# Optimization experiments

Hardware: AMD Instinct MI355X
Metric: run time of the kernel (lower is better)

Reference implementation:

```python
import jax, jax.numpy as jnp
import numpy as np

B, S, U, H = 4, 1024, 1024, 16
D = U // H  # d_k = 64


def setup_inputs() -> dict:
    key = jax.random.key(0)
    ks = jax.random.split(key, 11)
    f = lambda k, sh: jax.random.normal(k, sh, dtype=jnp.float32) * 0.02
    # causal multiplicative mask, as commonly passed to this module
    mask = jnp.broadcast_to(jnp.tril(jnp.ones((S, S), jnp.float32)), (B, S, S))
    return {
        "query": f(ks[0], (B, S, U)),
        "key": f(ks[1], (B, S, U)),
        "value": f(ks[2], (B, S, U)),
        "mask": mask,
        "Wq": f(ks[3], (U, U)), "bq": jnp.zeros((U,), jnp.float32),
        "Wk": f(ks[4], (U, U)), "bk": jnp.zeros((U,), jnp.float32),
        "Wv": f(ks[5], (U, U)), "bv": jnp.zeros((U,), jnp.float32),
        "Wo": f(ks[6], (U, U)), "bo": jnp.zeros((U,), jnp.float32),
    }


def reference(query, key, value, mask, Wq, bq, Wk, bk, Wv, bv, Wo, bo):
    scale = 1.0 / np.sqrt(D).astype(np.float32)
    # project and split heads: torch's split(d_k,dim=2)+cat(dim=0) == reshape [B,S,H,D]
    def heads(x, W, b):
        return (x @ W + b).reshape(B, S, H, D)
    q = heads(query, Wq, bq)
    k = heads(key, Wk, bk)
    v = heads(value, Wv, bv)
    A = jnp.einsum('bqhd,bkhd->bhqk', q, k) * scale  # [B,H,S,S]
    m = mask[:, None, :, :]  # broadcast over heads (== mask.repeat(n_heads,1,1))
    A = A * m - 1e10 * (1.0 - m)  # multiplicative + additive masking
    A = jax.nn.softmax(A, axis=-1)
    # dropout p=0.0 -> identity
    out = jnp.einsum('bhqk,bkhd->bqhd', A, v).reshape(B, S, U)
    return out @ Wo + bo
```

## Files before the change

kernel.cpp:

```cpp
#include <hip/hip_runtime.h>
#include <hip/hip_bf16.h>

typedef unsigned short u16;
typedef __attribute__((ext_vector_type(8))) short bf16x8;
typedef __attribute__((ext_vector_type(4))) float f32x4;
constexpr size_t M1 = 1024 * 1024;

static __device__ __forceinline__ float bf2f(u16 u) {
    return __uint_as_float(((unsigned)u) << 16);
}
static __device__ __forceinline__ u16 f2bf(float f) {
    __hip_bfloat16 h = __float2bfloat16(f);
    return *reinterpret_cast<u16*>(&h);
}
static __device__ __forceinline__ void g2lds16(const void* g, void* l) {
    __builtin_amdgcn_global_load_lds(
        (const __attribute__((address_space(1))) unsigned int*)g,
        (__attribute__((address_space(3))) unsigned int*)l, 16, 0, 0);
}
static __device__ __forceinline__ f32x4 mfma16(bf16x8 a, bf16x8 b, f32x4 c) {
    return __builtin_amdgcn_mfma_f32_16x16x32_bf16(a, b, c, 0, 0, 0);
}
static __device__ __forceinline__ bf16x8 ldfrag(const u16* base, int chunk) {
    return *(const bf16x8*)((const char*)base + (size_t)chunk * 16);
}
static __device__ __forceinline__ float fexp2(float x) {
    return __builtin_amdgcn_exp2f(x);
}

__global__ void sniff_kernel(const u16* __restrict__ q, int* __restrict__ flag) {
    const int i = threadIdx.x;
    const int e = (q[i] >> 7) & 0xFF;
    const unsigned long long m = __ballot(e >= 130);
    if (i == 0) *flag = (__popcll(m) >= 2) ? 1 : 0;
}

struct CastArgs { const float* src[2]; u16* dst[2]; int nChunks; };

__global__ __launch_bounds__(256) void cast_bf16(CastArgs ca, const int* __restrict__ flag) {
    if (*flag == 0) return;
    const int total = ca.nChunks;
    for (int c = blockIdx.x * 256 + threadIdx.x; c < total; c += gridDim.x * 256) {
        const int t = c >> 19;
        const size_t off = (size_t)(c & 524287);
        const float4 v0 = *((const float4*)ca.src[t] + off * 2);
        const float4 v1 = *((const float4*)ca.src[t] + off * 2 + 1);
        int4 v; u16* pv = (u16*)&v;
        pv[0] = f2bf(v0.x); pv[1] = f2bf(v0.y); pv[2] = f2bf(v0.z); pv[3] = f2bf(v0.w);
        pv[4] = f2bf(v1.x); pv[5] = f2bf(v1.y); pv[6] = f2bf(v1.z); pv[7] = f2bf(v1.w);
        *((int4*)ca.dst[t] + off) = v;
    }
}

struct T4 { const void* src[4]; u16* dst[4]; };

__global__ __launch_bounds__(256) void transpose64(
    T4 ta, const int* __restrict__ flag, int xRaw)
{
    __shared__ u16 Ts[64][72];
    const void* src = ta.src[blockIdx.z];
    u16* dst = ta.dst[blockIdx.z];
    const int tid = threadIdx.x;
    const int r0 = blockIdx.x * 64;
    const int c0 = blockIdx.y * 64;
    const bool f = xRaw && (*flag != 0);
#pragma unroll
    for (int i = 0; i < 4; ++i) {
        const int idx = tid + i * 256;
        const int r = idx >> 4, c4 = (idx & 15) * 4;
        if (f) {
            const float4 v = *(const float4*)((const float*)src + (size_t)(r0 + r) * 1024 + c0 + c4);
            Ts[r][c4 + 0] = f2bf(v.x); Ts[r][c4 + 1] = f2bf(v.y);
            Ts[r][c4 + 2] = f2bf(v.z); Ts[r][c4 + 3] = f2bf(v.w);
        } else {
            const ushort4 v = *(const ushort4*)((const u16*)src + (size_t)(r0 + r) * 1024 + c0 + c4);
            Ts[r][c4 + 0] = v.x; Ts[r][c4 + 1] = v.y;
            Ts[r][c4 + 2] = v.z; Ts[r][c4 + 3] = v.w;
        }
    }
    __syncthreads();
#pragma unroll
    for (int i = 0; i < 4; ++i) {
        const int idx = tid + i * 256;
        const int r = idx >> 4, c4 = (idx & 15) * 4;
        ushort4 o;
        o.x = Ts[c4 + 0][r]; o.y = Ts[c4 + 1][r];
        o.z = Ts[c4 + 2][r]; o.w = Ts[c4 + 3][r];
        *(ushort4*)(dst + (size_t)(c0 + r) * 1024 + r0 + c4) = o;
    }
}

struct G1 { const void* X; const u16* Xc; const u16* Wt; const void* Bias; void* Y; int yMode; };
struct G3 { G1 g[3]; };

union GS8 {
    struct { u16 A[2][2][128 * 64]; u16 B[2][2][128 * 64]; } st;
    u16 C[256 * 256];
};

__global__ __launch_bounds__(512, 2) void gemm256(
    G3 args, const int* __restrict__ flag)
{
    __shared__ __align__(16) GS8 sm;
    const G1 g = args.g[blockIdx.z];
    const bool f = (*flag != 0);
    const bool regA = f && (g.Xc == nullptr);
    const int tid = threadIdx.x;
    const int lane = tid & 63, w = tid >> 6;
    const int quad = lane >> 4, l16 = lane & 15;
    const int wr = w >> 2, wc = w & 3;
    const int rowBase = blockIdx.x * 256, colBase = blockIdx.y * 256;

    const u16* Xb = f ? g.Xc : (const u16*)g.X;
    const float* Xf = (const float*)g.X;

    f32x4 acc[8][4];
#pragma unroll
    for (int i = 0; i < 8; ++i)
#pragma unroll
        for (int j = 0; j < 4; ++j)
            acc[i][j] = f32x4{0.f, 0.f, 0.f, 0.f};

    auto stA = [&](int bf2, int h, int T2) {
        if (!regA) {
#pragma unroll
            for (int c = 0; c < 2; ++c) {
                const int l = c * 512 + tid;
                const int r  = ((l >> 6) << 3) | (l & 7);
                const int kc = (l >> 3) & 7;
                g2lds16(Xb + (size_t)(rowBase + h * 128 + r) * 1024 + T2 * 64 + kc * 8,
                        (char*)sm.st.A[bf2][h] + (size_t)l * 16);
            }
        } else {
#pragma unroll
            for (int c = 0; c < 2; ++c) {
                const int l = c * 512 + tid;
                const int r  = ((l >> 6) << 3) | (l & 7);
                const int kc = (l >> 3) & 7;
                const float* p = Xf + (size_t)(rowBase + h * 128 + r) * 1024 + T2 * 64 + kc * 8;
                const float4 v0 = *(const float4*)p;
                const float4 v1 = *(const float4*)(p + 4);
                int4 v; u16* pv = (u16*)&v;
                pv[0] = f2bf(v0.x); pv[1] = f2bf(v0.y); pv[2] = f2bf(v0.z); pv[3] = f2bf(v0.w);
                pv[4] = f2bf(v1.x); pv[5] = f2bf(v1.y); pv[6] = f2bf(v1.z); pv[7] = f2bf(v1.w);
                *(int4*)((char*)sm.st.A[bf2][h] + (size_t)l * 16) = v;
            }
            __builtin_amdgcn_s_waitcnt(0xC07F);
        }
    };
    auto stB = [&](int bf2, int h, int T2) {
#pragma unroll
        for (int c = 0; c < 2; ++c) {
            const int l = c * 512 + tid;
            const int r  = ((l >> 6) << 3) | (l & 7);
            const int kc = (l >> 3) & 7;
            g2lds16(g.Wt + (size_t)(colBase + h * 128 + r) * 1024 + T2 * 64 + kc * 8,
                    (char*)sm.st.B[bf2][h] + (size_t)l * 16);
        }
    };

    stA(0, 0, 0); stA(0, 1, 0); stB(0, 0, 0); stB(0, 1, 0);
    stA(1, 0, 1); stA(1, 1, 1); stB(1, 0, 1); stB(1, 1, 1);
    if (regA) __builtin_amdgcn_s_waitcnt(0x0074);
    else      __builtin_amdgcn_s_waitcnt(0x0078);
    __builtin_amdgcn_s_barrier();

    bf16x8 a[4][2], b[4][2];
    const int rbB = (wc & 1) * 64;

#pragma unroll 1
    for (int T = 0; T < 16; ++T) {
        const int buf = T & 1, nb = buf ^ 1;
        const u16* Ab = sm.st.A[buf][wr];
        const u16* Bb = sm.st.B[buf][wc >> 1];

#pragma unroll
        for (int i = 0; i < 4; ++i)
#pragma unroll
            for (int ks = 0; ks < 2; ++ks) {
                const int rl = i * 16 + l16;
                a[i][ks] = ldfrag(Ab, ((rl >> 3) << 6) | ((ks * 4 + quad) << 3) | (rl & 7));
            }
#pragma unroll
        for (int j = 0; j < 2; ++j)
#pragma unroll
            for (int ks = 0; ks < 2; ++ks) {
                const int rl = rbB + j * 16 + l16;
                b[j][ks] = ldfrag(Bb, ((rl >> 3) << 6) | ((ks * 4 + quad) << 3) | (rl & 7));
            }
        if (T >= 1 && T <= 14) stA(nb, 0, T + 1);
        __builtin_amdgcn_s_barrier();
        __builtin_amdgcn_s_setprio(1);
#pragma unroll
        for (int ks = 0; ks < 2; ++ks)
#pragma unroll
            for (int i = 0; i < 4; ++i)
#pragma unroll
                for (int j = 0; j < 2; ++j)
                    acc[i][j] = mfma16(a[i][ks], b[j][ks], acc[i][j]);
        __builtin_amdgcn_s_setprio(0);
        __builtin_amdgcn_s_barrier();

#pragma unroll
        for (int j = 2; j < 4; ++j)
#pragma unroll
            for (int ks = 0; ks < 2; ++ks) {
                const int rl = rbB + j * 16 + l16;
                b[j][ks] = ldfrag(Bb, ((rl >> 3) << 6) | ((ks * 4 + quad) << 3) | (rl & 7));
            }
        if (T >= 1 && T <= 14) stA(nb, 1, T + 1);
        __builtin_amdgcn_s_barrier();
        __builtin_amdgcn_s_setprio(1);
#pragma unroll
        for (int ks = 0; ks < 2; ++ks)
#pragma unroll
            for (int i = 0; i < 4; ++i)
#pragma unroll
                for (int j = 2; j < 4; ++j)
                    acc[i][j] = mfma16(a[i][ks], b[j][ks], acc[i][j]);
        __builtin_amdgcn_s_setprio(0);
        __builtin_amdgcn_s_barrier();

#pragma unroll
        for (int i = 0; i < 4; ++i)
#pragma unroll
            for (int ks = 0; ks < 2; ++ks) {
                const int rl = (i + 4) * 16 + l16;
                a[i][ks] = ldfrag(Ab, ((rl >> 3) << 6) | ((ks * 4 + quad) << 3) | (rl & 7));
            }
        if (T <= 13) stB(buf, 0, T + 2);
        __builtin_amdgcn_s_barrier();
        __builtin_amdgcn_s_setprio(1);
#pragma unroll
        for (int ks = 0; ks < 2; ++ks)
#pragma unroll
            for (int i = 0; i < 4; ++i)
#pragma unroll
                for (int j = 2; j < 4; ++j)
                    acc[i + 4][j] = mfma16(a[i][ks], b[j][ks], acc[i + 4][j]);
        __builtin_amdgcn_s_setprio(0);
        __builtin_amdgcn_s_barrier();

        if (T <= 13) stB(buf, 1, T + 2);
        __builtin_amdgcn_s_barrier();
        __builtin_amdgcn_s_setprio(1);
#pragma unroll
        for (int ks = 0; ks < 2; ++ks)
#pragma unroll
            for (int i = 0; i < 4; ++i)
#pragma unroll
                for (int j = 0; j < 2; ++j)
                    acc[i + 4][j] = mfma16(a[i][ks], b[j][ks], acc[i + 4][j]);
        __builtin_amdgcn_s_setprio(0);
        if (T < 14) __builtin_amdgcn_s_waitcnt(0x0074);
        else        __builtin_amdgcn_s_waitcnt(0x0070);
        __builtin_amdgcn_s_barrier();
    }

    const bool yf = (g.yMode == 2) && f;
    if (yf) {
#pragma unroll
        for (int j = 0; j < 4; ++j) {
            const int col = colBase + wc * 64 + j * 16 + l16;
            const float bv = ((const float*)g.Bias)[col];
#pragma unroll
            for (int i = 0; i < 8; ++i)
#pragma unroll
                for (int reg = 0; reg < 4; ++reg) {
                    const int row = rowBase + wr * 128 + i * 16 + quad * 4 + reg;
                    ((float*)g.Y)[(size_t)row * 1024 + col] = acc[i][j][reg] + bv;
                }
        }
        return;
    }

    __syncthreads();
    const bool vmode = (g.yMode == 1);
#pragma unroll
    for (int j = 0; j < 4; ++j) {
        const int cl = wc * 64 + j * 16 + l16;
        const float bv = f ? ((const float*)g.Bias)[colBase + cl]
                           : bf2f(((const u16*)g.Bias)[colBase + cl]);
#pragma unroll
        for (int i = 0; i < 8; ++i)
#pragma unroll
            for (int reg = 0; reg < 4; ++reg) {
                const int rl = wr * 128 + i * 16 + quad * 4 + reg;
                const int R = vmode ? cl : rl;
                const int Cc = vmode ? rl : cl;
                const int idx = R * 256 + ((((Cc >> 3) ^ (R & 31)) << 3) | (Cc & 7));
                sm.C[idx] = f2bf(acc[i][j][reg] + bv);
            }
    }
    __syncthreads();

    const int rr = tid >> 1, half = tid & 1;
    u16* dst;
    if (vmode) {
        const int bb = rowBase >> 10, s0 = rowBase & 1023;
        dst = (u16*)g.Y + (size_t)bb * M1 + (size_t)(colBase + rr) * 1024 + s0 + half * 128;
    } else {
        dst = (u16*)g.Y + (size_t)(rowBase + rr) * 1024 + colBase + half * 128;
    }
#pragma unroll
    for (int k2 = 0; k2 < 16; ++k2) {
        const int chunk = half * 16 + k2;
        const int4 v = *(const int4*)(sm.C + rr * 256 + ((chunk ^ (rr & 31)) << 3));
        *(int4*)(dst + k2 * 8) = v;
    }
}

union GSMem {
    struct { u16 A[3][128 * 32]; u16 B[3][128 * 32]; } st;
    u16 C[128 * 128];
};

__global__ __launch_bounds__(256) void gemm_mfma(
    G3 args, const int* __restrict__ flag, int xRaw)
{
    __shared__ __align__(16) GSMem sm;
    const G1 g = args.g[blockIdx.z];
    const bool f  = (*flag != 0);
    const bool xf = xRaw && f;
    const int tid = threadIdx.x;
    const int lane = tid & 63, w = tid >> 6;
    const int quad = lane >> 4, l16 = lane & 15;
    const int wm = (w & 1) * 64, wn = (w >> 1) * 64;
    const int rowBase = blockIdx.x * 128, colBase = blockIdx.y * 128;

    const u16* Xp = (const u16*)g.X;
    const float* Xf = (const float*)g.X;

    f32x4 acc[4][4];
#pragma unroll
    for (int i = 0; i < 4; ++i)
#pragma unroll
        for (int j = 0; j < 4; ++j)
            acc[i][j] = f32x4{0.f, 0.f, 0.f, 0.f};

    auto stage = [&](int buf, int k0) {
#pragma unroll
        for (int c = 0; c < 2; ++c) {
            const int l = c * 256 + tid;
            const int r = ((l >> 5) << 3) | (l & 7);
            const int kc = (l >> 3) & 3;
            g2lds16(g.Wt + (size_t)(colBase + r) * 1024 + k0 + kc * 8,
                    (char*)sm.st.B[buf] + (size_t)l * 16);
        }
        if (!xf) {
#pragma unroll
            for (int c = 0; c < 2; ++c) {
                const int l = c * 256 + tid;
                const int r = ((l >> 5) << 3) | (l & 7);
                const int kc = (l >> 3) & 3;
                g2lds16(Xp + (size_t)(rowBase + r) * 1024 + k0 + kc * 8,
                        (char*)sm.st.A[buf] + (size_t)l * 16);
            }
        } else {
#pragma unroll
            for (int c = 0; c < 2; ++c) {
                const int l = c * 256 + tid;
                const int r = ((l >> 5) << 3) | (l & 7);
                const int kc = (l >> 3) & 3;
                const float* p = Xf + (size_t)(rowBase + r) * 1024 + k0 + kc * 8;
                const float4 v0 = *(const float4*)p;
                const float4 v1 = *(const float4*)(p + 4);
                int4 v;
                u16* pv = (u16*)&v;
                pv[0] = f2bf(v0.x); pv[1] = f2bf(v0.y); pv[2] = f2bf(v0.z); pv[3] = f2bf(v0.w);
                pv[4] = f2bf(v1.x); pv[5] = f2bf(v1.y); pv[6] = f2bf(v1.z); pv[7] = f2bf(v1.w);
                *(int4*)((char*)sm.st.A[buf] + (size_t)l * 16) = v;
            }
        }
    };

    auto compute = [&](int buf) {
        bf16x8 a[4], b[4];
#pragma unroll
        for (int i = 0; i < 4; ++i) {
            const int r = wm + i * 16 + l16;
            a[i] = ldfrag(sm.st.A[buf], ((r >> 3) << 5) | (quad << 3) | (r & 7));
        }
#pragma unroll
        for (int j = 0; j < 4; ++j) {
            const int r = wn + j * 16 + l16;
            b[j] = ldfrag(sm.st.B[buf], ((r >> 3) << 5) | (quad << 3) | (r & 7));
        }
#pragma unroll
        for (int i = 0; i < 4; ++i)
#pragma unroll
            for (int j = 0; j < 4; ++j)
                acc[i][j] = mfma16(a[i], b[j], acc[i][j]);
    };

    stage(0, 0);
    stage(1, 32);
#pragma unroll 1
    for (int t = 0; t < 31; ++t) {
        __builtin_amdgcn_s_waitcnt(0x0074);
        __builtin_amdgcn_s_barrier();
        if (t + 2 < 32) stage((t + 2) % 3, (t + 2) * 32);
        compute(t % 3);
    }
    __builtin_amdgcn_s_waitcnt(0x0070);
    __builtin_amdgcn_s_barrier();
    compute(31 % 3);

    const bool yf = (g.yMode == 2) && f;
    if (yf) {
#pragma unroll
        for (int j = 0; j < 4; ++j) {
            const int col = colBase + wn + j * 16 + l16;
            const float bv = ((const float*)g.Bias)[col];
#pragma unroll
            for (int i = 0; i < 4; ++i)
#pragma unroll
                for (int reg = 0; reg < 4; ++reg) {
                    const int row = rowBase + wm + i * 16 + quad * 4 + reg;
                    ((float*)g.Y)[(size_t)row * 1024 + col] = acc[i][j][reg] + bv;
                }
        }
        return;
    }

    __syncthreads();
    const bool vmode = (g.yMode == 1);
#pragma unroll
    for (int j = 0; j < 4; ++j) {
        const int cl = wn + j * 16 + l16;
        const float bv = f ? ((const float*)g.Bias)[colBase + cl]
                           : bf2f(((const u16*)g.Bias)[colBase + cl]);
#pragma unroll
        for (int i = 0; i < 4; ++i)
#pragma unroll
            for (int reg = 0; reg < 4; ++reg) {
                const int rl = wm + i * 16 + quad * 4 + reg;
                const int R = vmode ? cl : rl;
                const int Cc = vmode ? rl : cl;
                const int idx = R * 128 + ((((Cc >> 3) ^ (R & 15)) << 3) | (Cc & 7));
                sm.C[idx] = f2bf(acc[i][j][reg] + bv);
            }
    }
    __syncthreads();

    const int rr = tid >> 1, half = tid & 1;
    u16* dst;
    if (vmode) {
        const int bb = rowBase >> 10, s0 = rowBase & 1023;
        dst = (u16*)g.Y + (size_t)bb * M1 + (size_t)(colBase + rr) * 1024 + s0 + half * 64;
    } else {
        dst = (u16*)g.Y + (size_t)(rowBase + rr) * 1024 + colBase + half * 64;
    }
#pragma unroll
    for (int k2 = 0; k2 < 8; ++k2) {
        const int chunk = half * 8 + k2;
        const int4 v = *(const int4*)(sm.C + rr * 128 + ((chunk ^ (rr & 15)) << 3));
        *(int4*)(dst + k2 * 8) = v;
    }
}

static __device__ __forceinline__ void attn_strip(
    const u16* __restrict__ Ks, const u16* __restrict__ Vs,
    u16* __restrict__ psw, const bf16x8* aq,
    float* m_run, float* l_run, f32x4* O,
    int w, int quad, int l16, bool diag)
{
    f32x4 s[4];
#pragma unroll
    for (int j = 0; j < 4; ++j) {
        const int r = j * 16 + l16;
        const bf16x8 b0 = ldfrag(Ks, ((r >> 3) << 6) | (quad << 3) | (r & 7));
        const bf16x8 b1 = ldfrag(Ks, ((r >> 3) << 6) | ((4 + quad) << 3) | (r & 7));
        f32x4 z = f32x4{0.f, 0.f, 0.f, 0.f};
        z = mfma16(aq[0], b0, z);
        s[j] = mfma16(aq[1], b1, z);
    }

    const float SC2 = 0.125f * 1.44269504089f;
    const int qrow0 = w * 16 + quad * 4;
#pragma unroll
    for (int j = 0; j < 4; ++j) {
        const int key = j * 16 + l16;
#pragma unroll
        for (int reg = 0; reg < 4; ++reg) {
            float v = s[j][reg] * SC2;
            if (diag && key > qrow0 + reg) v = -1e30f;
            s[j][reg] = v;
        }
    }

    float alpha[4];
#pragma unroll
    for (int reg = 0; reg < 4; ++reg) {
        float mx = fmaxf(fmaxf(s[0][reg], s[1][reg]), fmaxf(s[2][reg], s[3][reg]));
#pragma unroll
        for (int d = 1; d < 16; d <<= 1)
            mx = fmaxf(mx, __shfl_xor(mx, d));
        const float m_new = fmaxf(m_run[reg], mx);
        alpha[reg] = fexp2(m_run[reg] - m_new);
        float sm = 0.f;
#pragma unroll
        for (int j = 0; j < 4; ++j) {
            const float p = fexp2(s[j][reg] - m_new);
            s[j][reg] = p;
            sm += p;
        }
#pragma unroll
        for (int d = 1; d < 16; d <<= 1)
            sm += __shfl_xor(sm, d);
        l_run[reg] = l_run[reg] * alpha[reg] + sm;
        m_run[reg] = m_new;
    }

#pragma unroll
    for (int j = 0; j < 4; ++j)
#pragma unroll
        for (int reg = 0; reg < 4; ++reg)
            psw[(quad * 4 + reg) * 72 + j * 16 + l16] = f2bf(s[j][reg]);

#pragma unroll
    for (int j = 0; j < 4; ++j)
#pragma unroll
        for (int reg = 0; reg < 4; ++reg)
            O[j][reg] *= alpha[reg];

    bf16x8 ap[2];
#pragma unroll
    for (int kt = 0; kt < 2; ++kt)
        ap[kt] = *(const bf16x8*)((const char*)psw + (size_t)l16 * 144 + kt * 64 + quad * 16);
#pragma unroll
    for (int j = 0; j < 4; ++j) {
        const int r = j * 16 + l16;
        const bf16x8 b0 = ldfrag(Vs, ((r >> 3) << 6) | (quad << 3) | (r & 7));
        const bf16x8 b1 = ldfrag(Vs, ((r >> 3) << 6) | ((4 + quad) << 3) | (r & 7));
        O[j] = mfma16(ap[0], b0, O[j]);
        O[j] = mfma16(ap[1], b1, O[j]);
    }
}

__global__ __launch_bounds__(256) void attn_mfma(
    u16* __restrict__ qw, const u16* __restrict__ kw, const u16* __restrict__ vt)
{
    __shared__ __align__(16) u16 QA[64 * 64];
    __shared__ __align__(16) u16 QB[64 * 64];
    __shared__ __align__(16) u16 Ks[2][64 * 64];
    __shared__ __align__(16) u16 Vs[2][64 * 64];
    __shared__ __align__(16) u16 Ps[4][16 * 72];

    const int tid = threadIdx.x;
    const int lane = tid & 63, w = tid >> 6;
    const int quad = lane >> 4, l16 = lane & 15;
    const int qp = blockIdx.x, bh = blockIdx.y;
    const int b = bh >> 4, h = bh & 15;
    const int qtA = qp, qtB = 15 - qp;

    const u16* qgA = qw + (size_t)(b * 1024 + qtA * 64) * 1024 + h * 64;
    const u16* qgB = qw + (size_t)(b * 1024 + qtB * 64) * 1024 + h * 64;
    const u16* kg0 = kw + (size_t)(b * 1024) * 1024 + h * 64;
    const u16* vg0 = vt + (size_t)b * M1 + (size_t)(h * 64) * 1024;

    auto stageKV = [&](int buf, int kb) {
#pragma unroll
        for (int c = 0; c < 2; ++c) {
            const int l = c * 256 + tid;
            const int r = ((l >> 6) << 3) | (l & 7);
            const int kc = (l >> 3) & 7;
            g2lds16(kg0 + (size_t)(kb + r) * 1024 + kc * 8, (char*)Ks[buf] + (size_t)l * 16);
            g2lds16(vg0 + (size_t)r * 1024 + kb + kc * 8,   (char*)Vs[buf] + (size_t)l * 16);
        }
    };

#pragma unroll
    for (int c = 0; c < 2; ++c) {
        const int l = c * 256 + tid;
        const int r = ((l >> 6) << 3) | (l & 7);
        const int kc = (l >> 3) & 7;
        g2lds16(qgA + (size_t)r * 1024 + kc * 8, (char*)QA + (size_t)l * 16);
        g2lds16(qgB + (size_t)r * 1024 + kc * 8, (char*)QB + (size_t)l * 16);
    }
    stageKV(0, 0);
    __syncthreads();

    bf16x8 aqA[2], aqB[2];
    {
        const int r = w * 16 + l16;
#pragma unroll
        for (int kt = 0; kt < 2; ++kt) {
            aqA[kt] = ldfrag(QA, ((r >> 3) << 6) | ((kt * 4 + quad) << 3) | (r & 7));
            aqB[kt] = ldfrag(QB, ((r >> 3) << 6) | ((kt * 4 + quad) << 3) | (r & 7));
        }
    }

    f32x4 OA[4], OB[4];
    float mA[4], lA[4], mB[4], lB[4];
#pragma unroll
    for (int j = 0; j < 4; ++j) {
        OA[j] = f32x4{0.f, 0.f, 0.f, 0.f};
        OB[j] = f32x4{0.f, 0.f, 0.f, 0.f};
        mA[j] = -1e30f; lA[j] = 0.f;
        mB[j] = -1e30f; lB[j] = 0.f;
    }
    u16* psw = Ps[w];

    int cur = 0;
    for (int t = 0; t <= qtB; ++t) {
        if (t < qtB) stageKV(cur ^ 1, (t + 1) * 64);
        attn_strip(Ks[cur], Vs[cur], psw, aqB, mB, lB, OB, w, quad, l16, t == qtB);
        if (t <= qtA)
            attn_strip(Ks[cur], Vs[cur], psw, aqA, mA, lA, OA, w, quad, l16, t == qtA);
        __syncthreads();
        cur ^= 1;
    }

#pragma unroll
    for (int half = 0; half < 2; ++half) {
        const int qt = half ? qtB : qtA;
        const float* lr = half ? lB : lA;
        const f32x4* O = half ? OB : OA;
        u16* og = qw + (size_t)(b * 1024 + qt * 64 + w * 16 + quad * 4) * 1024 + h * 64;
#pragma unroll
        for (int reg = 0; reg < 4; ++reg) {
            const float inv = 1.f / lr[reg];
#pragma unroll
            for (int j = 0; j < 4; ++j)
                og[(size_t)reg * 1024 + j * 16 + l16] = f2bf(O[j][reg] * inv);
        }
    }
}

extern "C" void kernel_launch(void* const* d_in, const int* in_sizes, int n_in,
                              void* d_out, int out_size, void* d_ws, size_t ws_size,
                              hipStream_t stream)
{
    const void* query = d_in[0];
    const void* key   = d_in[1];
    const void* value = d_in[2];
    const void* Wq = d_in[4];
    const void* bq = d_in[5];
    const void* Wk = d_in[6];
    const void* bk = d_in[7];
    const void* Wv = d_in[8];
    const void* bv = d_in[9];
    const void* Wo = d_in[10];
    const void* bo = d_in[11];

    u16* qw   = (u16*)d_ws;
    u16* kw   = qw + 4 * M1;
    u16* vt   = qw + 8 * M1;
    u16* wt_o = qw + 12 * M1;
    u16* wt_q = qw + 13 * M1;
    u16* wt_k = qw + 14 * M1;
    u16* wt_v = qw + 15 * M1;
    int* flag = (int*)(qw + 16 * M1);

    u16* xq = (u16*)d_out;
    u16* xk = xq + 4 * M1;

    sniff_kernel<<<1, 64, 0, stream>>>((const u16*)query, flag);

    T4 wT; wT.src[0] = Wq; wT.src[1] = Wk; wT.src[2] = Wv; wT.src[3] = Wo;
    wT.dst[0] = wt_q; wT.dst[1] = wt_k; wT.dst[2] = wt_v; wT.dst[3] = wt_o;
    transpose64<<<dim3(16, 16, 4), 256, 0, stream>>>(wT, flag, 1);

    CastArgs cqk;
    cqk.src[0] = (const float*)query; cqk.src[1] = (const float*)key;
    cqk.dst[0] = xq; cqk.dst[1] = xk;
    cqk.nChunks = 2 * 524288;
    cast_bf16<<<2048, 256, 0, stream>>>(cqk, flag);

    G3 qkv;
    qkv.g[0] = G1{query, xq,      wt_q, bq, qw, 0};
    qkv.g[1] = G1{key,   xk,      wt_k, bk, kw, 0};
    qkv.g[2] = G1{value, nullptr, wt_v, bv, vt, 1};
    gemm256<<<dim3(16, 4, 3), 512, 0, stream>>>(qkv, flag);

    attn_mfma<<<dim3(8, 64), 256, 0, stream>>>(qw, kw, vt);

    G3 og;
    og.g[0] = G1{qw, nullptr, wt_o, bo, d_out, 2};
    og.g[1] = og.g[0]; og.g[2] = og.g[0];
    gemm_mfma<<<dim3(32, 8, 1), 256, 0, stream>>>(og, flag, 0);
}
```

Measured before the change: 269.2 us.

## Fuse fp32-to-bf16 input cast into QKV GEMM with register-prefetched A tiles

Drops the separate cast kernel for query and key, so all three projections read fp32 activations straight into the GEMM. The A-tile loads move into registers two k-steps ahead and are converted and written to shared memory later in the iteration. This avoids a synchronous wait after each load and hides global latency behind the MFMA phases. In exchange it needs more registers (and may lower occupancy), and the A operand is now read as fp32, so each GEMM reads more bytes.

```diff
diff --git a/kernel.cpp b/kernel.cpp
--- a/kernel.cpp
+++ b/kernel.cpp
@@ -33,23 +33,6 @@
     const int e = (q[i] >> 7) & 0xFF;
     const unsigned long long m = __ballot(e >= 130);
     if (i == 0) *flag = (__popcll(m) >= 2) ? 1 : 0;
-}
-
-struct CastArgs { const float* src[2]; u16* dst[2]; int nChunks; };
-
-__global__ __launch_bounds__(256) void cast_bf16(CastArgs ca, const int* __restrict__ flag) {
-    if (*flag == 0) return;
-    const int total = ca.nChunks;
-    for (int c = blockIdx.x * 256 + threadIdx.x; c < total; c += gridDim.x * 256) {
-        const int t = c >> 19;
-        const size_t off = (size_t)(c & 524287);
-        const float4 v0 = *((const float4*)ca.src[t] + off * 2);
-        const float4 v1 = *((const float4*)ca.src[t] + off * 2 + 1);
-        int4 v; u16* pv = (u16*)&v;
-        pv[0] = f2bf(v0.x); pv[1] = f2bf(v0.y); pv[2] = f2bf(v0.z); pv[3] = f2bf(v0.w);
-        pv[4] = f2bf(v1.x); pv[5] = f2bf(v1.y); pv[6] = f2bf(v1.z); pv[7] = f2bf(v1.w);
-        *((int4*)ca.dst[t] + off) = v;
-    }
 }
 
 struct T4 { const void* src[4]; u16* dst[4]; };
@@ -104,14 +87,14 @@
     __shared__ __align__(16) GS8 sm;
     const G1 g = args.g[blockIdx.z];
     const bool f = (*flag != 0);
-    const bool regA = f && (g.Xc == nullptr);
+    const bool regA = f;
     const int tid = threadIdx.x;
     const int lane = tid & 63, w = tid >> 6;
     const int quad = lane >> 4, l16 = lane & 15;
     const int wr = w >> 2, wc = w & 3;
     const int rowBase = blockIdx.x * 256, colBase = blockIdx.y * 256;
 
-    const u16* Xb = f ? g.Xc : (const u16*)g.X;
+    const u16* Xb = (const u16*)g.X;
     const float* Xf = (const float*)g.X;
 
     f32x4 acc[8][4];
@@ -122,30 +105,13 @@
             acc[i][j] = f32x4{0.f, 0.f, 0.f, 0.f};
 
     auto stA = [&](int bf2, int h, int T2) {
-        if (!regA) {
-#pragma unroll
-            for (int c = 0; c < 2; ++c) {
-                const int l = c * 512 + tid;
-                const int r  = ((l >> 6) << 3) | (l & 7);
-                const int kc = (l >> 3) & 7;
-                g2lds16(Xb + (size_t)(rowBase + h * 128 + r) * 1024 + T2 * 64 + kc * 8,
-                        (char*)sm.st.A[bf2][h] + (size_t)l * 16);
-            }
-        } else {
-#pragma unroll
-            for (int c = 0; c < 2; ++c) {
-                const int l = c * 512 + tid;
-                const int r  = ((l >> 6) << 3) | (l & 7);
-                const int kc = (l >> 3) & 7;
-                const float* p = Xf + (size_t)(rowBase + h * 128 + r) * 1024 + T2 * 64 + kc * 8;
-                const float4 v0 = *(const float4*)p;
-                const float4 v1 = *(const float4*)(p + 4);
-                int4 v; u16* pv = (u16*)&v;
-                pv[0] = f2bf(v0.x); pv[1] = f2bf(v0.y); pv[2] = f2bf(v0.z); pv[3] = f2bf(v0.w);
-                pv[4] = f2bf(v1.x); pv[5] = f2bf(v1.y); pv[6] = f2bf(v1.z); pv[7] = f2bf(v1.w);
-                *(int4*)((char*)sm.st.A[bf2][h] + (size_t)l * 16) = v;
-            }
-            __builtin_amdgcn_s_waitcnt(0xC07F);
+#pragma unroll
+        for (int c = 0; c < 2; ++c) {
+            const int l = c * 512 + tid;
+            const int r  = ((l >> 6) << 3) | (l & 7);
+            const int kc = (l >> 3) & 7;
+            g2lds16(Xb + (size_t)(rowBase + h * 128 + r) * 1024 + T2 * 64 + kc * 8,
+                    (char*)sm.st.A[bf2][h] + (size_t)l * 16);
         }
     };
     auto stB = [&](int bf2, int h, int T2) {
@@ -159,13 +125,45 @@
         }
     };
 
-    stA(0, 0, 0); stA(0, 1, 0); stB(0, 0, 0); stB(0, 1, 0);
-    stA(1, 0, 1); stA(1, 1, 1); stB(1, 0, 1); stB(1, 1, 1);
-    if (regA) __builtin_amdgcn_s_waitcnt(0x0074);
-    else      __builtin_amdgcn_s_waitcnt(0x0078);
+    if (regA) {
+#pragma unroll
+        for (int t2 = 0; t2 < 2; ++t2) {
+            float4 ld[2][2][2];
+#pragma unroll
+            for (int h = 0; h < 2; ++h)
+#pragma unroll
+                for (int c = 0; c < 2; ++c) {
+                    const int l = c * 512 + tid;
+                    const int r  = ((l >> 6) << 3) | (l & 7);
+                    const int kc = (l >> 3) & 7;
+                    const float* p = Xf + (size_t)(rowBase + h * 128 + r) * 1024 + t2 * 64 + kc * 8;
+                    ld[h][c][0] = *(const float4*)p;
+                    ld[h][c][1] = *(const float4*)(p + 4);
+                }
+#pragma unroll
+            for (int h = 0; h < 2; ++h)
+#pragma unroll
+                for (int c = 0; c < 2; ++c) {
+                    const int l = c * 512 + tid;
+                    int4 v; u16* pv = (u16*)&v;
+                    pv[0] = f2bf(ld[h][c][0].x); pv[1] = f2bf(ld[h][c][0].y);
+                    pv[2] = f2bf(ld[h][c][0].z); pv[3] = f2bf(ld[h][c][0].w);
+                    pv[4] = f2bf(ld[h][c][1].x); pv[5] = f2bf(ld[h][c][1].y);
+                    pv[6] = f2bf(ld[h][c][1].z); pv[7] = f2bf(ld[h][c][1].w);
+                    *(int4*)((char*)sm.st.A[t2][h] + (size_t)l * 16) = v;
+                }
+        }
+        stB(0, 0, 0); stB(0, 1, 0); stB(1, 0, 1); stB(1, 1, 1);
+        __builtin_amdgcn_s_waitcnt(0x0074);
+    } else {
+        stA(0, 0, 0); stA(0, 1, 0); stB(0, 0, 0); stB(0, 1, 0);
+        stA(1, 0, 1); stA(1, 1, 1); stB(1, 0, 1); stB(1, 1, 1);
+        __builtin_amdgcn_s_waitcnt(0x0078);
+    }
     __builtin_amdgcn_s_barrier();
 
     bf16x8 a[4][2], b[4][2];
+    float4 ra[2][2][2];
     const int rbB = (wc & 1) * 64;
 
 #pragma unroll 1
@@ -188,7 +186,7 @@
                 const int rl = rbB + j * 16 + l16;
                 b[j][ks] = ldfrag(Bb, ((rl >> 3) << 6) | ((ks * 4 + quad) << 3) | (rl & 7));
             }
-        if (T >= 1 && T <= 14) stA(nb, 0, T + 1);
+        if (!regA && T >= 1 && T <= 14) stA(nb, 0, T + 1);
         __builtin_amdgcn_s_barrier();
         __builtin_amdgcn_s_setprio(1);
 #pragma unroll
@@ -208,7 +206,7 @@
                 const int rl = rbB + j * 16 + l16;
                 b[j][ks] = ldfrag(Bb, ((rl >> 3) << 6) | ((ks * 4 + quad) << 3) | (rl & 7));
             }
-        if (T >= 1 && T <= 14) stA(nb, 1, T + 1);
+        if (!regA && T >= 1 && T <= 14) stA(nb, 1, T + 1);
         __builtin_amdgcn_s_barrier();
         __builtin_amdgcn_s_setprio(1);
 #pragma unroll
@@ -228,6 +226,18 @@
                 const int rl = (i + 4) * 16 + l16;
                 a[i][ks] = ldfrag(Ab, ((rl >> 3) << 6) | ((ks * 4 + quad) << 3) | (rl & 7));
             }
+        if (regA && T >= 1 && T <= 14) {
+#pragma unroll
+            for (int c = 0; c < 2; ++c) {
+                const int l = c * 512 + tid;
+                int4 v; u16* pv = (u16*)&v;
+                pv[0] = f2bf(ra[0][c][0].x); pv[1] = f2bf(ra[0][c][0].y);
+                pv[2] = f2bf(ra[0][c][0].z); pv[3] = f2bf(ra[0][c][0].w);
+                pv[4] = f2bf(ra[0][c][1].x); pv[5] = f2bf(ra[0][c][1].y);
+                pv[6] = f2bf(ra[0][c][1].z); pv[7] = f2bf(ra[0][c][1].w);
+                *(int4*)((char*)sm.st.A[nb][0] + (size_t)l * 16) = v;
+            }
+        }
         if (T <= 13) stB(buf, 0, T + 2);
         __builtin_amdgcn_s_barrier();
         __builtin_amdgcn_s_setprio(1);
@@ -241,7 +251,36 @@
         __builtin_amdgcn_s_setprio(0);
         __builtin_amdgcn_s_barrier();
 
+        if (regA) {
+            if (T >= 1 && T <= 14) {
+#pragma unroll
+                for (int c = 0; c < 2; ++c) {
+                    const int l = c * 512 + tid;
+                    int4 v; u16* pv = (u16*)&v;
+                    pv[0] = f2bf(ra[1][c][0].x); pv[1] = f2bf(ra[1][c][0].y);
+                    pv[2] = f2bf(ra[1][c][0].z); pv[3] = f2bf(ra[1][c][0].w);
+                    pv[4] = f2bf(ra[1][c][1].x); pv[5] = f2bf(ra[1][c][1].y);
+                    pv[6] = f2bf(ra[1][c][1].z); pv[7] = f2bf(ra[1][c][1].w);
+                    *(int4*)((char*)sm.st.A[nb][1] + (size_t)l * 16) = v;
+                }
+            }
+            if (T <= 13) {
+#pragma unroll
+                for (int h = 0; h < 2; ++h)
+#pragma unroll
+                    for (int c = 0; c < 2; ++c) {
+                        const int l = c * 512 + tid;
+                        const int r  = ((l >> 6) << 3) | (l & 7);
+                        const int kc = (l >> 3) & 7;
+                        const float* p = Xf + (size_t)(rowBase + h * 128 + r) * 1024
+                                            + (T + 2) * 64 + kc * 8;
+                        ra[h][c][0] = *(const float4*)p;
+                        ra[h][c][1] = *(const float4*)(p + 4);
+                    }
+            }
+        }
         if (T <= 13) stB(buf, 1, T + 2);
+        __builtin_amdgcn_sched_barrier(0);
         __builtin_amdgcn_s_barrier();
         __builtin_amdgcn_s_setprio(1);
 #pragma unroll
@@ -252,8 +291,12 @@
                 for (int j = 0; j < 2; ++j)
                     acc[i + 4][j] = mfma16(a[i][ks], b[j][ks], acc[i + 4][j]);
         __builtin_amdgcn_s_setprio(0);
-        if (T < 14) __builtin_amdgcn_s_waitcnt(0x0074);
-        else        __builtin_amdgcn_s_waitcnt(0x0070);
+        if (T < 14) {
+            if (regA) __builtin_amdgcn_s_waitcnt(0x007C);
+            else      __builtin_amdgcn_s_waitcnt(0x0074);
+        } else {
+            __builtin_amdgcn_s_waitcnt(0x0070);
+        }
         __builtin_amdgcn_s_barrier();
     }
 
@@ -653,24 +696,15 @@
     u16* wt_v = qw + 15 * M1;
     int* flag = (int*)(qw + 16 * M1);
 
-    u16* xq = (u16*)d_out;
-    u16* xk = xq + 4 * M1;
-
     sniff_kernel<<<1, 64, 0, stream>>>((const u16*)query, flag);
 
     T4 wT; wT.src[0] = Wq; wT.src[1] = Wk; wT.src[2] = Wv; wT.src[3] = Wo;
     wT.dst[0] = wt_q; wT.dst[1] = wt_k; wT.dst[2] = wt_v; wT.dst[3] = wt_o;
     transpose64<<<dim3(16, 16, 4), 256, 0, stream>>>(wT, flag, 1);
 
-    CastArgs cqk;
-    cqk.src[0] = (const float*)query; cqk.src[1] = (const float*)key;
-    cqk.dst[0] = xq; cqk.dst[1] = xk;
-    cqk.nChunks = 2 * 524288;
-    cast_bf16<<<2048, 256, 0, stream>>>(cqk, flag);
-
     G3 qkv;
-    qkv.g[0] = G1{query, xq,      wt_q, bq, qw, 0};
-    qkv.g[1] = G1{key,   xk,      wt_k, bk, kw, 0};
+    qkv.g[0] = G1{query, nullptr, wt_q, bq, qw, 0};
+    qkv.g[1] = G1{key,   nullptr, wt_k, bk, kw, 0};
     qkv.g[2] = G1{value, nullptr, wt_v, bv, vt, 1};
     gemm256<<<dim3(16, 4, 3), 512, 0, stream>>>(qkv, flag);
 
```

Result: faster. 261.4 us (-2.9%).
